# Kernel optimization log

Hardware: AMD Instinct MI355X
Metric: run time of the kernel (lower is better)

Reference implementation:

```python
import jax, jax.numpy as jnp
import numpy as np

C = 512          # channels
NH = 8           # num_heads
ENC = 512        # encoder_channels
SCALE_P = 1.0    # channels_scale_for_positional_embedding
CP = int(C * SCALE_P)
GROUPS = 32


def group_norm(x, g, b, eps=1e-5):
    # x: (N, C, L); GroupNorm32 computes stats in fp32
    N, Ch, L = x.shape
    xg = x.reshape(N, GROUPS, Ch // GROUPS, L).astype(jnp.float32)
    mu = xg.mean(axis=(2, 3), keepdims=True)
    var = xg.var(axis=(2, 3), keepdims=True)
    xn = ((xg - mu) * jax.lax.rsqrt(var + eps)).reshape(N, Ch, L).astype(x.dtype)
    return xn * g[None, :, None] + b[None, :, None]


def conv1(x, W, b):
    # 1x1 conv1d: x (N, Cin, L), W (Cout, Cin), b (Cout)
    return jnp.einsum('oc,ncl->nol', W, x) + b[None, :, None]


def setup_inputs() -> dict:
    key = jax.random.key(0)
    ks = iter(jax.random.split(key, 40))
    rn = lambda *s: jax.random.normal(next(ks), s, dtype=jnp.float32)
    inp = {
        'x': rn(8, C, 32, 32),
        'xf_out': rn(8, ENC, 64),
        'obj_contour_embedding': rn(8, ENC, 64),
        'obj_description_embedding': rn(8, ENC, 64),
        'image_patch_contour_embedding': rn(8, ENC, 1024),
        # norm_for_qkv
        'gn_qkv_g': jnp.ones(C), 'gn_qkv_b': jnp.zeros(C),
        # projectors (1x1 conv weights); zero_module proj_out given random weights for a meaningful baseline
        'W_self_qkv': rn(3 * C, C) * 0.02, 'b_self_qkv': jnp.zeros(3 * C),
        'W_cross_q': rn(C, C) * 0.02, 'b_cross_q': jnp.zeros(C),
        'W_content': rn(2 * C, ENC) * 0.02, 'b_content': jnp.zeros(2 * C),
        'W_pos': rn(CP, ENC) * 0.02, 'b_pos': jnp.zeros(CP),
        'gn_desc_g': jnp.ones(ENC), 'gn_desc_b': jnp.zeros(ENC),
        'gn_cpos_g': jnp.ones(CP), 'gn_cpos_b': jnp.zeros(CP),
        'gn_ipos_g': jnp.ones(CP), 'gn_ipos_b': jnp.zeros(CP),
        'W_self_out': rn(C, C) * 0.02, 'b_self_out': jnp.zeros(C),
        'W_cross_out': rn(C, C) * 0.02, 'b_cross_out': jnp.zeros(C),
    }
    return inp


def _attn(q, k, v, scale):
    # q,k: (B, Cq, T/S), v: (B, Cv, S)
    w = jnp.einsum('bct,bcs->bts', q * scale, k * scale)
    w = jax.nn.softmax(w.astype(jnp.float32), axis=-1).astype(q.dtype)
    return jnp.einsum('bts,bcs->bct', w, v)


def reference(x, xf_out, obj_contour_embedding, obj_description_embedding,
              image_patch_contour_embedding,
              gn_qkv_g, gn_qkv_b, W_self_qkv, b_self_qkv, W_cross_q, b_cross_q,
              W_content, b_content, W_pos, b_pos,
              gn_desc_g, gn_desc_b, gn_cpos_g, gn_cpos_b, gn_ipos_g, gn_ipos_b,
              W_self_out, b_self_out, W_cross_out, b_cross_out):
    b_, c_, h_, w_ = x.shape
    xf = x.reshape(b_, c_, -1)                      # (N, C, L1)
    L1 = xf.shape[-1]
    L2 = obj_contour_embedding.shape[-1]
    dc = C // NH
    dp = CP // NH
    scale = float(int((1 + SCALE_P) * C) // NH) ** -0.25

    # ---- self-attention over image patches ----
    qkv = conv1(group_norm(xf, gn_qkv_g, gn_qkv_b), W_self_qkv, b_self_qkv)
    sq, sk, sv = jnp.split(qkv, 3, axis=1)
    sq = sq.reshape(b_ * NH, dc, L1)
    sk = sk.reshape(b_ * NH, dc, L1)
    sv = sv.reshape(b_ * NH, dc, L1)

    ipos = conv1(image_patch_contour_embedding, W_pos, b_pos)
    ipos = group_norm(ipos, gn_ipos_g, gn_ipos_b)
    ipos = ipos.reshape(b_ * NH, dp, L1)

    sq = jnp.concatenate([sq, ipos], axis=1)
    sk = jnp.concatenate([sk, ipos], axis=1)
    self_out = _attn(sq, sk, sv, scale).reshape(b_, C, L1)
    self_out = conv1(self_out, W_self_out, b_self_out)
    xf = xf + self_out

    # ---- cross-attention to object tokens ----
    cq = conv1(group_norm(xf, gn_qkv_g, gn_qkv_b), W_cross_q, b_cross_q)
    cq = cq.reshape(b_ * NH, dc, L1)
    cq = jnp.concatenate([cq, ipos], axis=1)

    cpos = conv1(obj_contour_embedding, W_pos, b_pos)
    cpos = group_norm(cpos, gn_cpos_g, gn_cpos_b)
    cpos = cpos.reshape(b_ * NH, dp, L2)

    content = (xf_out + group_norm(obj_description_embedding, gn_desc_g, gn_desc_b)) / 2
    kv = conv1(content, W_content, b_content)
    ck, cv = jnp.split(kv, 2, axis=1)
    ck = ck.reshape(b_ * NH, dc, L2)
    cv = cv.reshape(b_ * NH, dc, L2)
    ck = jnp.concatenate([ck, cpos], axis=1)

    cross_out = _attn(cq, ck, cv, scale).reshape(b_, C, L1)
    cross_out = conv1(cross_out, W_cross_out, b_cross_out)

    return (xf + cross_out).reshape(b_, c_, h_, w_)
```

## Files before the change

### kernel.cpp

```cpp
#include <hip/hip_runtime.h>

typedef unsigned short u16;
typedef __attribute__((ext_vector_type(8))) short bf16x8;
typedef __attribute__((ext_vector_type(4))) float f32x4;

__device__ __forceinline__ float bf2f(u16 u) {
  union { unsigned int i; float f; } v;
  v.i = ((unsigned int)u) << 16;
  return v.f;
}
__device__ __forceinline__ u16 f2bf(float f) {
  union { float f; unsigned int i; } v;
  v.f = f;
  unsigned int r = v.i + 0x7FFFu + ((v.i >> 16) & 1u);
  return (u16)(r >> 16);
}
__device__ __forceinline__ unsigned int cvtpk(float lo, float hi) {
  unsigned int r;
  asm("v_cvt_pk_bf16_f32 %0, %1, %2" : "=v"(r) : "v"(lo), "v"(hi));
  return r;
}

__device__ __forceinline__ float4 ld4f(const float* p) {
  return *reinterpret_cast<const float4*>(p);
}
__device__ __forceinline__ float4 ld4f(const u16* p) {
  uint2 v = *reinterpret_cast<const uint2*>(p);
  float4 r;
  r.x = bf2f((u16)(v.x & 0xffff)); r.y = bf2f((u16)(v.x >> 16));
  r.z = bf2f((u16)(v.y & 0xffff)); r.w = bf2f((u16)(v.y >> 16));
  return r;
}

template <typename TIN>
__global__ __launch_bounds__(1024) void gn_kernel(
    const TIN* __restrict__ In, u16* __restrict__ OutBuf,
    const float* __restrict__ G, const float* __restrict__ Bt,
    const float* __restrict__ Add, float post_scale,
    int C, int L, int cpg)
{
  const int blk = blockIdx.x;
  const int n = blk >> 5, grp = blk & 31;
  const size_t base = ((size_t)n * C + (size_t)grp * cpg) * L;
  const int cnt = cpg * L;
  const int cnt4 = cnt >> 2;
  const int tid = threadIdx.x;

  float s = 0.f, s2 = 0.f;
  for (int i = tid; i < cnt4; i += 1024) {
    float4 v = ld4f(In + base + (size_t)i * 4);
    s += v.x + v.y + v.z + v.w;
    s2 += v.x * v.x + v.y * v.y + v.z * v.z + v.w * v.w;
  }
#pragma unroll
  for (int d = 1; d < 64; d <<= 1) {
    s += __shfl_xor(s, d);
    s2 += __shfl_xor(s2, d);
  }
  __shared__ float ps[16], ps2[16], stat[2];
  const int wid = tid >> 6;
  if ((tid & 63) == 0) { ps[wid] = s; ps2[wid] = s2; }
  __syncthreads();
  if (tid == 0) {
    float a = 0.f, b2 = 0.f;
#pragma unroll
    for (int w = 0; w < 16; ++w) { a += ps[w]; b2 += ps2[w]; }
    const float mean = a / cnt;
    const float var = b2 / cnt - mean * mean;
    stat[0] = mean;
    stat[1] = rsqrtf(var + 1e-5f);
  }
  __syncthreads();
  const float mean = stat[0], rstd = stat[1];

  for (int i = tid; i < cnt4; i += 1024) {
    const int i4 = i * 4;
    const int ch = grp * cpg + i4 / L;
    float4 v = ld4f(In + base + i4);
    const float g = G[ch] * rstd, bt = Bt[ch] - mean * rstd * G[ch];
    float4 r;
    r.x = v.x * g + bt; r.y = v.y * g + bt;
    r.z = v.z * g + bt; r.w = v.w * g + bt;
    if (Add) {
      float4 a = *reinterpret_cast<const float4*>(Add + base + i4);
      r.x = (r.x + a.x) * post_scale; r.y = (r.y + a.y) * post_scale;
      r.z = (r.z + a.z) * post_scale; r.w = (r.w + a.w) * post_scale;
    }
    uint2 o;
    o.x = (unsigned int)f2bf(r.x) | ((unsigned int)f2bf(r.y) << 16);
    o.y = (unsigned int)f2bf(r.z) | ((unsigned int)f2bf(r.w) << 16);
    *reinterpret_cast<uint2*>(OutBuf + base + i4) = o;
  }
}

__device__ __forceinline__ void load4(const u16* p, u16* d) {
  uint2 v = *reinterpret_cast<const uint2*>(p);
  d[0] = (u16)(v.x & 0xffff); d[1] = (u16)(v.x >> 16);
  d[2] = (u16)(v.y & 0xffff); d[3] = (u16)(v.y >> 16);
}
__device__ __forceinline__ void load4(const float* p, u16* d) {
  float4 v = *reinterpret_cast<const float4*>(p);
  d[0] = f2bf(v.x); d[1] = f2bf(v.y); d[2] = f2bf(v.z); d[3] = f2bf(v.w);
}
__device__ __forceinline__ void load8(const u16* p, u16* d) {
  union { uint4 q; u16 u[8]; } t;
  t.q = *reinterpret_cast<const uint4*>(p);
#pragma unroll
  for (int i = 0; i < 8; ++i) d[i] = t.u[i];
}

template <typename TX, int LT>
__global__ __launch_bounds__(256) void gemm_conv(
    const TX* __restrict__ X, const float* __restrict__ W,
    const float* __restrict__ Bias,
    u16* __restrict__ OutBf, float* __restrict__ Out32,
    const float* __restrict__ Res,
    int Cin, int L, int O, int mode)
{
  constexpr int NL = LT / 16;
  __shared__ __align__(16) u16 As[64][40];
  __shared__ __align__(16) u16 Bs[LT][40];
  const int tid = threadIdx.x;
  const int wave = tid >> 6;
  const int lane = tid & 63;
  const int n = blockIdx.z;
  const int o0 = blockIdx.x * 64;
  const int l0 = blockIdx.y * LT;
  const TX* Xn = X + (size_t)n * Cin * L;

  const int ao = tid >> 2, akc = (tid & 3) * 8;
  const int c2 = (tid & 15) * 2, lt0 = (tid >> 4) * NL;
  const float* wp = W + (size_t)(o0 + ao) * Cin + akc;
  const TX* xp0 = Xn + (size_t)c2 * L + l0 + lt0;
  const TX* xp1 = xp0 + L;

  f32x4 acc[NL];
#pragma unroll
  for (int i = 0; i < NL; ++i) acc[i] = (f32x4){0.f, 0.f, 0.f, 0.f};

  const int row = lane & 15;
  const int kh = (lane >> 4) * 8;

  float4 wa = *reinterpret_cast<const float4*>(wp);
  float4 wb = *reinterpret_cast<const float4*>(wp + 4);
  u16 blo[NL], bhi[NL];
#pragma unroll
  for (int ch = 0; ch < NL; ch += 4) {
    load4(xp0 + ch, blo + ch);
    load4(xp1 + ch, bhi + ch);
  }

  const int nK = Cin >> 5;
  for (int kt = 0; kt < nK; ++kt) {
    {
      union { uint4 q; u16 u[8]; } ap;
      ap.u[0] = f2bf(wa.x); ap.u[1] = f2bf(wa.y);
      ap.u[2] = f2bf(wa.z); ap.u[3] = f2bf(wa.w);
      ap.u[4] = f2bf(wb.x); ap.u[5] = f2bf(wb.y);
      ap.u[6] = f2bf(wb.z); ap.u[7] = f2bf(wb.w);
      *reinterpret_cast<uint4*>(&As[ao][akc]) = ap.q;
    }
#pragma unroll
    for (int j = 0; j < NL; ++j)
      *reinterpret_cast<unsigned int*>(&Bs[lt0 + j][c2]) =
          (unsigned int)blo[j] | ((unsigned int)bhi[j] << 16);
    __syncthreads();

    if (kt + 1 < nK) {
      const int k0 = (kt + 1) * 32;
      wa = *reinterpret_cast<const float4*>(wp + k0);
      wb = *reinterpret_cast<const float4*>(wp + k0 + 4);
#pragma unroll
      for (int ch = 0; ch < NL; ch += 4) {
        load4(xp0 + (size_t)k0 * L + ch, blo + ch);
        load4(xp1 + (size_t)k0 * L + ch, bhi + ch);
      }
    }

    bf16x8 a = *reinterpret_cast<const bf16x8*>(&As[wave * 16 + row][kh]);
#pragma unroll
    for (int lt = 0; lt < NL; ++lt) {
      bf16x8 b = *reinterpret_cast<const bf16x8*>(&Bs[lt * 16 + row][kh]);
      acc[lt] = __builtin_amdgcn_mfma_f32_16x16x32_bf16(a, b, acc[lt], 0, 0, 0);
    }
    __syncthreads();
  }

  const int col = lane & 15;
  const int r0 = (lane >> 4) * 4;
#pragma unroll
  for (int lt = 0; lt < NL; ++lt) {
    const int ll = l0 + lt * 16 + col;
#pragma unroll
    for (int j = 0; j < 4; ++j) {
      const int oo = o0 + wave * 16 + r0 + j;
      float v = acc[lt][j] + Bias[oo];
      const size_t idx = ((size_t)n * O + oo) * L + ll;
      if (mode == 1) {
        Out32[idx] = v + Res[idx];
      } else {
        OutBf[idx] = f2bf(v);
      }
    }
  }
}

__global__ __launch_bounds__(256) void gemm_qkv(
    const u16* __restrict__ X, const float* __restrict__ W,
    const float* __restrict__ Bias, u16* __restrict__ OutBf,
    int Cin, int L, int O)
{
  __shared__ __align__(16) u16 As[128][40];
  __shared__ __align__(16) u16 Bs[128][40];
  const int tid = threadIdx.x;
  const int wave = tid >> 6;
  const int lane = tid & 63;
  const int n = blockIdx.z;
  const int o0 = blockIdx.x * 128;
  const int l0 = blockIdx.y * 128;
  const u16* Xn = X + (size_t)n * Cin * L;

  const int ao = tid >> 1, ak = (tid & 1) * 16;
  const int c2 = (tid & 15) * 2, lt0 = (tid >> 4) * 8;
  const float* wp = W + (size_t)(o0 + ao) * Cin + ak;
  const u16* xp0 = Xn + (size_t)c2 * L + l0 + lt0;
  const u16* xp1 = xp0 + L;

  f32x4 acc[2][8];
#pragma unroll
  for (int g = 0; g < 2; ++g)
#pragma unroll
    for (int i = 0; i < 8; ++i) acc[g][i] = (f32x4){0.f, 0.f, 0.f, 0.f};

  const int row = lane & 15;
  const int kh = (lane >> 4) * 8;

  float4 w0 = *reinterpret_cast<const float4*>(wp);
  float4 w1 = *reinterpret_cast<const float4*>(wp + 4);
  float4 w2 = *reinterpret_cast<const float4*>(wp + 8);
  float4 w3 = *reinterpret_cast<const float4*>(wp + 12);
  u16 blo[8], bhi[8];
  load8(xp0, blo);
  load8(xp1, bhi);

  const int nK = Cin >> 5;
  for (int kt = 0; kt < nK; ++kt) {
    {
      union { uint4 q; u16 u[8]; } ap;
      ap.u[0] = f2bf(w0.x); ap.u[1] = f2bf(w0.y);
      ap.u[2] = f2bf(w0.z); ap.u[3] = f2bf(w0.w);
      ap.u[4] = f2bf(w1.x); ap.u[5] = f2bf(w1.y);
      ap.u[6] = f2bf(w1.z); ap.u[7] = f2bf(w1.w);
      *reinterpret_cast<uint4*>(&As[ao][ak]) = ap.q;
      ap.u[0] = f2bf(w2.x); ap.u[1] = f2bf(w2.y);
      ap.u[2] = f2bf(w2.z); ap.u[3] = f2bf(w2.w);
      ap.u[4] = f2bf(w3.x); ap.u[5] = f2bf(w3.y);
      ap.u[6] = f2bf(w3.z); ap.u[7] = f2bf(w3.w);
      *reinterpret_cast<uint4*>(&As[ao][ak + 8]) = ap.q;
    }
#pragma unroll
    for (int j = 0; j < 8; ++j)
      *reinterpret_cast<unsigned int*>(&Bs[lt0 + j][c2]) =
          (unsigned int)blo[j] | ((unsigned int)bhi[j] << 16);
    __syncthreads();

    if (kt + 1 < nK) {
      const int k0 = (kt + 1) * 32;
      w0 = *reinterpret_cast<const float4*>(wp + k0);
      w1 = *reinterpret_cast<const float4*>(wp + k0 + 4);
      w2 = *reinterpret_cast<const float4*>(wp + k0 + 8);
      w3 = *reinterpret_cast<const float4*>(wp + k0 + 12);
      load8(xp0 + (size_t)k0 * L, blo);
      load8(xp1 + (size_t)k0 * L, bhi);
    }

    bf16x8 a0 = *reinterpret_cast<const bf16x8*>(&As[wave * 32 + row][kh]);
    bf16x8 a1 = *reinterpret_cast<const bf16x8*>(&As[wave * 32 + 16 + row][kh]);
#pragma unroll
    for (int lt = 0; lt < 8; ++lt) {
      bf16x8 b = *reinterpret_cast<const bf16x8*>(&Bs[lt * 16 + row][kh]);
      acc[0][lt] = __builtin_amdgcn_mfma_f32_16x16x32_bf16(a0, b, acc[0][lt], 0, 0, 0);
      acc[1][lt] = __builtin_amdgcn_mfma_f32_16x16x32_bf16(a1, b, acc[1][lt], 0, 0, 0);
    }
    __syncthreads();
  }

  const int col = lane & 15;
  const int r0 = (lane >> 4) * 4;
#pragma unroll
  for (int g = 0; g < 2; ++g)
#pragma unroll
    for (int lt = 0; lt < 8; ++lt) {
      const int ll = l0 + lt * 16 + col;
#pragma unroll
      for (int j = 0; j < 4; ++j) {
        const int oo = o0 + wave * 32 + g * 16 + r0 + j;
        OutBf[((size_t)n * O + oo) * L + ll] = f2bf(acc[g][lt][j] + Bias[oo]);
      }
    }
}

__global__ __launch_bounds__(256, 2) void flash_attn(
    const u16* __restrict__ qA, int qA_C, int qA_off,
    const u16* __restrict__ qB,
    const u16* __restrict__ kA, int kA_C, int kA_off,
    const u16* __restrict__ kB,
    const u16* __restrict__ V, int v_C, int v_off,
    u16* __restrict__ Out, int S_len, float qscale)
{
  __shared__ __align__(16) u16 smem[20480];
  u16* const Qs = smem;
  u16* const Ks = smem;
  u16* const Ps = smem + 8192;
  u16* const Vt = smem + 16384;

  const int tid = threadIdx.x;
  const int wave = tid >> 6, lane = tid & 63;
  const int b = blockIdx.y >> 3, h = blockIdx.y & 7;
  const int t0 = blockIdx.x * 128;
  const int l16 = lane & 15, q4 = lane >> 4;
  const int swz = (l16 & 7) << 3;

  const int c2 = (tid & 63) * 2;
  const u16* q0 = (c2 < 64)
      ? qA + ((size_t)b * qA_C + qA_off + h * 64 + c2) * 1024 + t0
      : qB + ((size_t)b * 512 + h * 64 + (c2 - 64)) * 1024 + t0;
  const u16* q1 = q0 + 1024;
  const u16* k0 = (c2 < 64)
      ? kA + ((size_t)b * kA_C + kA_off + h * 64 + c2) * (size_t)S_len
      : kB + ((size_t)b * 512 + h * 64 + (c2 - 64)) * (size_t)S_len;
  const u16* k1 = k0 + S_len;
  const u16* vb = V + ((size_t)b * v_C + v_off + h * 64) * (size_t)S_len;

  const int s8 = (tid >> 6) * 8;
  const int cv0 = tid >> 3, sb0 = (tid & 7) * 8;
  const int cv1 = (tid + 256) >> 3, sb1 = sb0;

  uint4 kr0a = *reinterpret_cast<const uint4*>(k0 + s8);
  uint4 kr0c = *reinterpret_cast<const uint4*>(k1 + s8);
  uint4 kr1a = *reinterpret_cast<const uint4*>(k0 + s8 + 32);
  uint4 kr1c = *reinterpret_cast<const uint4*>(k1 + s8 + 32);
  uint4 vr0 = *reinterpret_cast<const uint4*>(vb + (size_t)cv0 * S_len + sb0);
  uint4 vr1 = *reinterpret_cast<const uint4*>(vb + (size_t)cv1 * S_len + sb1);

#pragma unroll
  for (int it = 0; it < 4; ++it) {
    const int t8 = (tid >> 6) * 8 + it * 32;
    union { uint4 q; u16 u[8]; } a, c;
    a.q = *reinterpret_cast<const uint4*>(q0 + t8);
    c.q = *reinterpret_cast<const uint4*>(q1 + t8);
#pragma unroll
    for (int j = 0; j < 8; ++j) {
      const unsigned int w =
          cvtpk(bf2f(a.u[j]) * qscale, bf2f(c.u[j]) * qscale);
      *reinterpret_cast<unsigned int*>(&Qs[(t8 + j) * 128 + (c2 ^ (j << 3))]) = w;
    }
  }
  __syncthreads();

  bf16x8 qf[2][4];
#pragma unroll
  for (int g = 0; g < 2; ++g)
#pragma unroll
    for (int kk = 0; kk < 4; ++kk)
      qf[g][kk] = *reinterpret_cast<const bf16x8*>(
          &Qs[(wave * 32 + g * 16 + l16) * 128 + ((kk * 32 + q4 * 8) ^ swz)]);
  __syncthreads();

  float m_run[2][4], l_run[2][4];
  f32x4 o_acc[2][4];
#pragma unroll
  for (int g = 0; g < 2; ++g)
#pragma unroll
    for (int j = 0; j < 4; ++j) {
      m_run[g][j] = -1e30f; l_run[g][j] = 0.f;
      o_acc[g][j] = (f32x4){0.f, 0.f, 0.f, 0.f};
    }

  const int NT = S_len >> 6;
  for (int t = 0; t < NT; ++t) {
    {
      union { uint4 q; u16 u[8]; } a, c;
      a.q = kr0a; c.q = kr0c;
#pragma unroll
      for (int j = 0; j < 8; ++j)
        *reinterpret_cast<unsigned int*>(&Ks[(s8 + j) * 128 + (c2 ^ (j << 3))]) =
            (unsigned int)a.u[j] | ((unsigned int)c.u[j] << 16);
      a.q = kr1a; c.q = kr1c;
#pragma unroll
      for (int j = 0; j < 8; ++j)
        *reinterpret_cast<unsigned int*>(&Ks[(s8 + 32 + j) * 128 + (c2 ^ (j << 3))]) =
            (unsigned int)a.u[j] | ((unsigned int)c.u[j] << 16);
    }
    *reinterpret_cast<uint4*>(&Vt[cv0 * 64 + (sb0 ^ ((cv0 & 7) << 3))]) = vr0;
    *reinterpret_cast<uint4*>(&Vt[cv1 * 64 + (sb1 ^ ((cv1 & 7) << 3))]) = vr1;
    __syncthreads();

    if (t + 1 < NT) {
      const int sc = (t + 1) * 64;
      kr0a = *reinterpret_cast<const uint4*>(k0 + sc + s8);
      kr0c = *reinterpret_cast<const uint4*>(k1 + sc + s8);
      kr1a = *reinterpret_cast<const uint4*>(k0 + sc + s8 + 32);
      kr1c = *reinterpret_cast<const uint4*>(k1 + sc + s8 + 32);
      vr0 = *reinterpret_cast<const uint4*>(vb + (size_t)cv0 * S_len + sc + sb0);
      vr1 = *reinterpret_cast<const uint4*>(vb + (size_t)cv1 * S_len + sc + sb1);
    }

    f32x4 sacc[2][4];
#pragma unroll
    for (int g = 0; g < 2; ++g)
#pragma unroll
      for (int st = 0; st < 4; ++st) sacc[g][st] = (f32x4){0.f, 0.f, 0.f, 0.f};
    __builtin_amdgcn_s_setprio(1);
#pragma unroll
    for (int st = 0; st < 4; ++st) {
#pragma unroll
      for (int kk = 0; kk < 4; ++kk) {
        bf16x8 kf = *reinterpret_cast<const bf16x8*>(
            &Ks[(st * 16 + l16) * 128 + ((kk * 32 + q4 * 8) ^ swz)]);
        sacc[0][st] = __builtin_amdgcn_mfma_f32_16x16x32_bf16(qf[0][kk], kf, sacc[0][st], 0, 0, 0);
        sacc[1][st] = __builtin_amdgcn_mfma_f32_16x16x32_bf16(qf[1][kk], kf, sacc[1][st], 0, 0, 0);
      }
    }
    __builtin_amdgcn_s_setprio(0);

    float mt[2][4];
#pragma unroll
    for (int g = 0; g < 2; ++g)
#pragma unroll
      for (int j = 0; j < 4; ++j)
        mt[g][j] = fmaxf(fmaxf(sacc[g][0][j], sacc[g][1][j]),
                         fmaxf(sacc[g][2][j], sacc[g][3][j]));

    bool grow = false;
#pragma unroll
    for (int g = 0; g < 2; ++g)
#pragma unroll
      for (int j = 0; j < 4; ++j)
        grow = grow || (mt[g][j] > m_run[g][j] + 8.f);
    if (__any(grow)) {
#pragma unroll
      for (int g = 0; g < 2; ++g) {
#pragma unroll
        for (int d = 1; d < 16; d <<= 1)
#pragma unroll
          for (int j = 0; j < 4; ++j)
            mt[g][j] = fmaxf(mt[g][j], __shfl_xor(mt[g][j], d));
#pragma unroll
        for (int j = 0; j < 4; ++j) {
          const float mn = fmaxf(m_run[g][j], mt[g][j]);
          const float corr = exp2f(m_run[g][j] - mn);
          m_run[g][j] = mn;
          l_run[g][j] *= corr;
#pragma unroll
          for (int ct = 0; ct < 4; ++ct) o_acc[g][ct][j] *= corr;
        }
      }
    }

#pragma unroll
    for (int g = 0; g < 2; ++g)
#pragma unroll
      for (int st = 0; st < 4; ++st)
#pragma unroll
        for (int j = 0; j < 4; ++j) {
          const float p = exp2f(sacc[g][st][j] - m_run[g][j]);
          l_run[g][j] += p;
          Ps[(wave * 32 + g * 16 + q4 * 4 + j) * 64 +
             ((st * 16 + l16) ^ (((q4 * 4 + j) & 7) << 3))] = f2bf(p);
        }

    bf16x8 pa[2][2];
#pragma unroll
    for (int g = 0; g < 2; ++g)
#pragma unroll
      for (int ks = 0; ks < 2; ++ks)
        pa[g][ks] = *reinterpret_cast<const bf16x8*>(
            &Ps[(wave * 32 + g * 16 + l16) * 64 + ((ks * 32 + q4 * 8) ^ swz)]);
    __builtin_amdgcn_s_setprio(1);
#pragma unroll
    for (int ct = 0; ct < 4; ++ct) {
#pragma unroll
      for (int ks = 0; ks < 2; ++ks) {
        bf16x8 vf = *reinterpret_cast<const bf16x8*>(
            &Vt[(ct * 16 + l16) * 64 + ((ks * 32 + q4 * 8) ^ swz)]);
        o_acc[0][ct] = __builtin_amdgcn_mfma_f32_16x16x32_bf16(pa[0][ks], vf, o_acc[0][ct], 0, 0, 0);
        o_acc[1][ct] = __builtin_amdgcn_mfma_f32_16x16x32_bf16(pa[1][ks], vf, o_acc[1][ct], 0, 0, 0);
      }
    }
    __builtin_amdgcn_s_setprio(0);
    __syncthreads();
  }

#pragma unroll
  for (int g = 0; g < 2; ++g) {
#pragma unroll
    for (int d = 1; d < 16; d <<= 1)
#pragma unroll
      for (int j = 0; j < 4; ++j) l_run[g][j] += __shfl_xor(l_run[g][j], d);
    float inv[4];
#pragma unroll
    for (int j = 0; j < 4; ++j) inv[j] = 1.f / l_run[g][j];
    const size_t obase =
        ((size_t)b * 512 + h * 64) * 1024 + t0 + wave * 32 + g * 16 + q4 * 4;
#pragma unroll
    for (int ct = 0; ct < 4; ++ct) {
      union { unsigned long long d; u16 u[4]; } pk;
#pragma unroll
      for (int j = 0; j < 4; ++j) pk.u[j] = f2bf(o_acc[g][ct][j] * inv[j]);
      *reinterpret_cast<unsigned long long*>(
          Out + obase + (size_t)(ct * 16 + l16) * 1024) = pk.d;
    }
  }
}

extern "C" void kernel_launch(void* const* d_in, const int* in_sizes, int n_in,
                              void* d_out, int out_size, void* d_ws, size_t ws_size,
                              hipStream_t stream) {
  const float* X_in        = (const float*)d_in[0];
  const float* xf_out      = (const float*)d_in[1];
  const float* obj_cont    = (const float*)d_in[2];
  const float* obj_desc    = (const float*)d_in[3];
  const float* ipce        = (const float*)d_in[4];
  const float* gn_qkv_g    = (const float*)d_in[5];
  const float* gn_qkv_b    = (const float*)d_in[6];
  const float* W_self_qkv  = (const float*)d_in[7];
  const float* b_self_qkv  = (const float*)d_in[8];
  const float* W_cross_q   = (const float*)d_in[9];
  const float* b_cross_q   = (const float*)d_in[10];
  const float* W_content   = (const float*)d_in[11];
  const float* b_content   = (const float*)d_in[12];
  const float* W_pos       = (const float*)d_in[13];
  const float* b_pos       = (const float*)d_in[14];
  const float* gn_desc_g   = (const float*)d_in[15];
  const float* gn_desc_b   = (const float*)d_in[16];
  const float* gn_cpos_g   = (const float*)d_in[17];
  const float* gn_cpos_b   = (const float*)d_in[18];
  const float* gn_ipos_g   = (const float*)d_in[19];
  const float* gn_ipos_b   = (const float*)d_in[20];
  const float* W_self_out  = (const float*)d_in[21];
  const float* b_self_out  = (const float*)d_in[22];
  const float* W_cross_out = (const float*)d_in[23];
  const float* b_cross_out = (const float*)d_in[24];

  char* base = (char*)d_ws;
  u16* A = (u16*)base;
  u16* B = (u16*)(base + 8 * 1024 * 1024);
  u16* C = (u16*)(base + 32 * 1024 * 1024);
  u16* D = (u16*)(base + 40 * 1024 * 1024);

  u16* norm1 = A;
  u16* norm2 = A;
  u16* cposr   = A;
  u16* cpos    = A + 262144;
  u16* content = A + 2 * 262144;
  u16* kvbuf   = A + 3 * 262144;
  u16* qkv  = B;
  u16* cq   = B;
  u16* ipos = C;
  u16* iposr = D;
  u16* attn1 = D;
  u16* cattn = D;
  float* xf32 = (float*)d_out;
  float* outp = (float*)d_out;

  const float qscale = 0.08838834764831845f * 1.4426950408889634f;
  dim3 blk(256);
  dim3 blkgn(1024);

  gn_kernel<float><<<dim3(256), blkgn, 0, stream>>>(X_in, norm1, gn_qkv_g, gn_qkv_b,
                                                    nullptr, 1.f, 512, 1024, 16);
  gemm_qkv<<<dim3(12, 8, 8), blk, 0, stream>>>(norm1, W_self_qkv, b_self_qkv,
                                               qkv, 512, 1024, 1536);
  gemm_conv<float, 128><<<dim3(8, 8, 8), blk, 0, stream>>>(ipce, W_pos, b_pos, iposr,
                                                           nullptr, nullptr,
                                                           512, 1024, 512, 0);
  gn_kernel<u16><<<dim3(256), blkgn, 0, stream>>>(iposr, ipos, gn_ipos_g, gn_ipos_b,
                                                  nullptr, 1.f, 512, 1024, 16);
  flash_attn<<<dim3(8, 64), blk, 0, stream>>>(qkv, 1536, 0, ipos,
                                              qkv, 1536, 512, ipos,
                                              qkv, 1536, 1024,
                                              attn1, 1024, qscale);
  gemm_conv<u16, 128><<<dim3(8, 8, 8), blk, 0, stream>>>(attn1, W_self_out, b_self_out,
                                                         nullptr, xf32, X_in,
                                                         512, 1024, 512, 1);
  gn_kernel<float><<<dim3(256), blkgn, 0, stream>>>(xf32, norm2, gn_qkv_g, gn_qkv_b,
                                                    nullptr, 1.f, 512, 1024, 16);
  gemm_conv<u16, 128><<<dim3(8, 8, 8), blk, 0, stream>>>(norm2, W_cross_q, b_cross_q, cq,
                                                         nullptr, nullptr,
                                                         512, 1024, 512, 0);
  gemm_conv<float, 64><<<dim3(8, 1, 8), blk, 0, stream>>>(obj_cont, W_pos, b_pos, cposr,
                                                          nullptr, nullptr,
                                                          512, 64, 512, 0);
  gn_kernel<u16><<<dim3(256), blkgn, 0, stream>>>(cposr, cpos, gn_cpos_g, gn_cpos_b,
                                                  nullptr, 1.f, 512, 64, 16);
  gn_kernel<float><<<dim3(256), blkgn, 0, stream>>>(obj_desc, content, gn_desc_g,
                                                    gn_desc_b, xf_out, 0.5f, 512, 64, 16);
  gemm_conv<u16, 64><<<dim3(16, 1, 8), blk, 0, stream>>>(content, W_content, b_content,
                                                         kvbuf, nullptr, nullptr,
                                                         512, 64, 1024, 0);
  flash_attn<<<dim3(8, 64), blk, 0, stream>>>(cq, 512, 0, ipos,
                                              kvbuf, 1024, 0, cpos,
                                              kvbuf, 1024, 512,
                                              cattn, 64, qscale);
  gemm_conv<u16, 128><<<dim3(8, 8, 8), blk, 0, stream>>>(cattn, W_cross_out, b_cross_out,
                                                         nullptr, outp, xf32,
                                                         512, 1024, 512, 1);
}
```

Measured before the change: 247.8 us.

## Use 512-thread flash attention blocks with one 16-row query group per wave

The flash attention kernel moves from 4 waves each owning 32 query rows to 8 waves each owning 16 rows, with 512 threads per block. The K, V and Q staging loads are spread over more threads, so each thread loads half as much. Per-thread register use for the accumulators and Q fragments roughly halves, which gives more waves in flight to hide latency. In exchange, each K/V fragment read from shared memory now feeds one MFMA instead of two, and more waves take part in each block barrier.

```diff
diff --git a/kernel.cpp b/kernel.cpp
--- a/kernel.cpp
+++ b/kernel.cpp
@@ -300,7 +300,7 @@
     }
 }
 
-__global__ __launch_bounds__(256, 2) void flash_attn(
+__global__ __launch_bounds__(512) void flash_attn(
     const u16* __restrict__ qA, int qA_C, int qA_off,
     const u16* __restrict__ qB,
     const u16* __restrict__ kA, int kA_C, int kA_off,
@@ -321,7 +321,7 @@
   const int l16 = lane & 15, q4 = lane >> 4;
   const int swz = (l16 & 7) << 3;
 
-  const int c2 = (tid & 63) * 2;
+  const int c2 = lane * 2;
   const u16* q0 = (c2 < 64)
       ? qA + ((size_t)b * qA_C + qA_off + h * 64 + c2) * 1024 + t0
       : qB + ((size_t)b * 512 + h * 64 + (c2 - 64)) * 1024 + t0;
@@ -332,20 +332,16 @@
   const u16* k1 = k0 + S_len;
   const u16* vb = V + ((size_t)b * v_C + v_off + h * 64) * (size_t)S_len;
 
-  const int s8 = (tid >> 6) * 8;
-  const int cv0 = tid >> 3, sb0 = (tid & 7) * 8;
-  const int cv1 = (tid + 256) >> 3, sb1 = sb0;
-
-  uint4 kr0a = *reinterpret_cast<const uint4*>(k0 + s8);
-  uint4 kr0c = *reinterpret_cast<const uint4*>(k1 + s8);
-  uint4 kr1a = *reinterpret_cast<const uint4*>(k0 + s8 + 32);
-  uint4 kr1c = *reinterpret_cast<const uint4*>(k1 + s8 + 32);
-  uint4 vr0 = *reinterpret_cast<const uint4*>(vb + (size_t)cv0 * S_len + sb0);
-  uint4 vr1 = *reinterpret_cast<const uint4*>(vb + (size_t)cv1 * S_len + sb1);
-
-#pragma unroll
-  for (int it = 0; it < 4; ++it) {
-    const int t8 = (tid >> 6) * 8 + it * 32;
+  const int s8 = wave * 8;
+  const int cv = tid >> 3, sb = (tid & 7) * 8;
+
+  uint4 kra = *reinterpret_cast<const uint4*>(k0 + s8);
+  uint4 krc = *reinterpret_cast<const uint4*>(k1 + s8);
+  uint4 vr = *reinterpret_cast<const uint4*>(vb + (size_t)cv * S_len + sb);
+
+#pragma unroll
+  for (int it = 0; it < 2; ++it) {
+    const int t8 = wave * 8 + it * 64;
     union { uint4 q; u16 u[8]; } a, c;
     a.q = *reinterpret_cast<const uint4*>(q0 + t8);
     c.q = *reinterpret_cast<const uint4*>(q1 + t8);
@@ -358,59 +354,44 @@
   }
   __syncthreads();
 
-  bf16x8 qf[2][4];
-#pragma unroll
-  for (int g = 0; g < 2; ++g)
-#pragma unroll
-    for (int kk = 0; kk < 4; ++kk)
-      qf[g][kk] = *reinterpret_cast<const bf16x8*>(
-          &Qs[(wave * 32 + g * 16 + l16) * 128 + ((kk * 32 + q4 * 8) ^ swz)]);
+  bf16x8 qf[4];
+#pragma unroll
+  for (int kk = 0; kk < 4; ++kk)
+    qf[kk] = *reinterpret_cast<const bf16x8*>(
+        &Qs[(wave * 16 + l16) * 128 + ((kk * 32 + q4 * 8) ^ swz)]);
   __syncthreads();
 
-  float m_run[2][4], l_run[2][4];
-  f32x4 o_acc[2][4];
-#pragma unroll
-  for (int g = 0; g < 2; ++g)
-#pragma unroll
-    for (int j = 0; j < 4; ++j) {
-      m_run[g][j] = -1e30f; l_run[g][j] = 0.f;
-      o_acc[g][j] = (f32x4){0.f, 0.f, 0.f, 0.f};
-    }
+  float m_run[4], l_run[4];
+  f32x4 o_acc[4];
+#pragma unroll
+  for (int j = 0; j < 4; ++j) {
+    m_run[j] = -1e30f; l_run[j] = 0.f;
+    o_acc[j] = (f32x4){0.f, 0.f, 0.f, 0.f};
+  }
 
   const int NT = S_len >> 6;
   for (int t = 0; t < NT; ++t) {
     {
       union { uint4 q; u16 u[8]; } a, c;
-      a.q = kr0a; c.q = kr0c;
+      a.q = kra; c.q = krc;
 #pragma unroll
       for (int j = 0; j < 8; ++j)
         *reinterpret_cast<unsigned int*>(&Ks[(s8 + j) * 128 + (c2 ^ (j << 3))]) =
             (unsigned int)a.u[j] | ((unsigned int)c.u[j] << 16);
-      a.q = kr1a; c.q = kr1c;
-#pragma unroll
-      for (int j = 0; j < 8; ++j)
-        *reinterpret_cast<unsigned int*>(&Ks[(s8 + 32 + j) * 128 + (c2 ^ (j << 3))]) =
-            (unsigned int)a.u[j] | ((unsigned int)c.u[j] << 16);
-    }
-    *reinterpret_cast<uint4*>(&Vt[cv0 * 64 + (sb0 ^ ((cv0 & 7) << 3))]) = vr0;
-    *reinterpret_cast<uint4*>(&Vt[cv1 * 64 + (sb1 ^ ((cv1 & 7) << 3))]) = vr1;
+    }
+    *reinterpret_cast<uint4*>(&Vt[cv * 64 + (sb ^ ((cv & 7) << 3))]) = vr;
     __syncthreads();
 
     if (t + 1 < NT) {
       const int sc = (t + 1) * 64;
-      kr0a = *reinterpret_cast<const uint4*>(k0 + sc + s8);
-      kr0c = *reinterpret_cast<const uint4*>(k1 + sc + s8);
-      kr1a = *reinterpret_cast<const uint4*>(k0 + sc + s8 + 32);
-      kr1c = *reinterpret_cast<const uint4*>(k1 + sc + s8 + 32);
-      vr0 = *reinterpret_cast<const uint4*>(vb + (size_t)cv0 * S_len + sc + sb0);
-      vr1 = *reinterpret_cast<const uint4*>(vb + (size_t)cv1 * S_len + sc + sb1);
-    }
-
-    f32x4 sacc[2][4];
-#pragma unroll
-    for (int g = 0; g < 2; ++g)
-#pragma unroll
-      for (int st = 0; st < 4; ++st) sacc[g][st] = (f32x4){0.f, 0.f, 0.f, 0.f};
+      kra = *reinterpret_cast<const uint4*>(k0 + sc + s8);
+      krc = *reinterpret_cast<const uint4*>(k1 + sc + s8);
+      vr = *reinterpret_cast<const uint4*>(vb + (size_t)cv * S_len + sc + sb);
+    }
+
+    f32x4 sacc[4];
+#pragma unroll
+    for (int st = 0; st < 4; ++st) sacc[st] = (f32x4){0.f, 0.f, 0.f, 0.f};
     __builtin_amdgcn_s_setprio(1);
 #pragma unroll
     for (int st = 0; st < 4; ++st) {
@@ -418,65 +399,53 @@
       for (int kk = 0; kk < 4; ++kk) {
         bf16x8 kf = *reinterpret_cast<const bf16x8*>(
             &Ks[(st * 16 + l16) * 128 + ((kk * 32 + q4 * 8) ^ swz)]);
-        sacc[0][st] = __builtin_amdgcn_mfma_f32_16x16x32_bf16(qf[0][kk], kf, sacc[0][st], 0, 0, 0);
-        sacc[1][st] = __builtin_amdgcn_mfma_f32_16x16x32_bf16(qf[1][kk], kf, sacc[1][st], 0, 0, 0);
+        sacc[st] = __builtin_amdgcn_mfma_f32_16x16x32_bf16(qf[kk], kf, sacc[st], 0, 0, 0);
       }
     }
     __builtin_amdgcn_s_setprio(0);
 
-    float mt[2][4];
-#pragma unroll
-    for (int g = 0; g < 2; ++g)
-#pragma unroll
-      for (int j = 0; j < 4; ++j)
-        mt[g][j] = fmaxf(fmaxf(sacc[g][0][j], sacc[g][1][j]),
-                         fmaxf(sacc[g][2][j], sacc[g][3][j]));
+    float mt[4];
+#pragma unroll
+    for (int j = 0; j < 4; ++j)
+      mt[j] = fmaxf(fmaxf(sacc[0][j], sacc[1][j]),
+                    fmaxf(sacc[2][j], sacc[3][j]));
 
     bool grow = false;
 #pragma unroll
-    for (int g = 0; g < 2; ++g)
-#pragma unroll
-      for (int j = 0; j < 4; ++j)
-        grow = grow || (mt[g][j] > m_run[g][j] + 8.f);
+    for (int j = 0; j < 4; ++j)
+      grow = grow || (mt[j] > m_run[j] + 8.f);
     if (__any(grow)) {
 #pragma unroll
-      for (int g = 0; g < 2; ++g) {
-#pragma unroll
-        for (int d = 1; d < 16; d <<= 1)
-#pragma unroll
-          for (int j = 0; j < 4; ++j)
-            mt[g][j] = fmaxf(mt[g][j], __shfl_xor(mt[g][j], d));
-#pragma unroll
-        for (int j = 0; j < 4; ++j) {
-          const float mn = fmaxf(m_run[g][j], mt[g][j]);
-          const float corr = exp2f(m_run[g][j] - mn);
-          m_run[g][j] = mn;
-          l_run[g][j] *= corr;
-#pragma unroll
-          for (int ct = 0; ct < 4; ++ct) o_acc[g][ct][j] *= corr;
-        }
-      }
-    }
-
-#pragma unroll
-    for (int g = 0; g < 2; ++g)
-#pragma unroll
-      for (int st = 0; st < 4; ++st)
-#pragma unroll
-        for (int j = 0; j < 4; ++j) {
-          const float p = exp2f(sacc[g][st][j] - m_run[g][j]);
-          l_run[g][j] += p;
-          Ps[(wave * 32 + g * 16 + q4 * 4 + j) * 64 +
-             ((st * 16 + l16) ^ (((q4 * 4 + j) & 7) << 3))] = f2bf(p);
-        }
-
-    bf16x8 pa[2][2];
-#pragma unroll
-    for (int g = 0; g < 2; ++g)
-#pragma unroll
-      for (int ks = 0; ks < 2; ++ks)
-        pa[g][ks] = *reinterpret_cast<const bf16x8*>(
-            &Ps[(wave * 32 + g * 16 + l16) * 64 + ((ks * 32 + q4 * 8) ^ swz)]);
+      for (int d = 1; d < 16; d <<= 1)
+#pragma unroll
+        for (int j = 0; j < 4; ++j)
+          mt[j] = fmaxf(mt[j], __shfl_xor(mt[j], d));
+#pragma unroll
+      for (int j = 0; j < 4; ++j) {
+        const float mn = fmaxf(m_run[j], mt[j]);
+        const float corr = exp2f(m_run[j] - mn);
+        m_run[j] = mn;
+        l_run[j] *= corr;
+#pragma unroll
+        for (int ct = 0; ct < 4; ++ct) o_acc[ct][j] *= corr;
+      }
+    }
+
+#pragma unroll
+    for (int st = 0; st < 4; ++st)
+#pragma unroll
+      for (int j = 0; j < 4; ++j) {
+        const float p = exp2f(sacc[st][j] - m_run[j]);
+        l_run[j] += p;
+        Ps[(wave * 16 + q4 * 4 + j) * 64 +
+           ((st * 16 + l16) ^ (((q4 * 4 + j) & 7) << 3))] = f2bf(p);
+      }
+
+    bf16x8 pa[2];
+#pragma unroll
+    for (int ks = 0; ks < 2; ++ks)
+      pa[ks] = *reinterpret_cast<const bf16x8*>(
+          &Ps[(wave * 16 + l16) * 64 + ((ks * 32 + q4 * 8) ^ swz)]);
     __builtin_amdgcn_s_setprio(1);
 #pragma unroll
     for (int ct = 0; ct < 4; ++ct) {
@@ -484,8 +453,7 @@
       for (int ks = 0; ks < 2; ++ks) {
         bf16x8 vf = *reinterpret_cast<const bf16x8*>(
             &Vt[(ct * 16 + l16) * 64 + ((ks * 32 + q4 * 8) ^ swz)]);
-        o_acc[0][ct] = __builtin_amdgcn_mfma_f32_16x16x32_bf16(pa[0][ks], vf, o_acc[0][ct], 0, 0, 0);
-        o_acc[1][ct] = __builtin_amdgcn_mfma_f32_16x16x32_bf16(pa[1][ks], vf, o_acc[1][ct], 0, 0, 0);
+        o_acc[ct] = __builtin_amdgcn_mfma_f32_16x16x32_bf16(pa[ks], vf, o_acc[ct], 0, 0, 0);
       }
     }
     __builtin_amdgcn_s_setprio(0);
@@ -493,24 +461,21 @@
   }
 
 #pragma unroll
-  for (int g = 0; g < 2; ++g) {
-#pragma unroll
-    for (int d = 1; d < 16; d <<= 1)
-#pragma unroll
-      for (int j = 0; j < 4; ++j) l_run[g][j] += __shfl_xor(l_run[g][j], d);
-    float inv[4];
-#pragma unroll
-    for (int j = 0; j < 4; ++j) inv[j] = 1.f / l_run[g][j];
-    const size_t obase =
-        ((size_t)b * 512 + h * 64) * 1024 + t0 + wave * 32 + g * 16 + q4 * 4;
-#pragma unroll
-    for (int ct = 0; ct < 4; ++ct) {
-      union { unsigned long long d; u16 u[4]; } pk;
-#pragma unroll
-      for (int j = 0; j < 4; ++j) pk.u[j] = f2bf(o_acc[g][ct][j] * inv[j]);
-      *reinterpret_cast<unsigned long long*>(
-          Out + obase + (size_t)(ct * 16 + l16) * 1024) = pk.d;
-    }
+  for (int d = 1; d < 16; d <<= 1)
+#pragma unroll
+    for (int j = 0; j < 4; ++j) l_run[j] += __shfl_xor(l_run[j], d);
+  float inv[4];
+#pragma unroll
+  for (int j = 0; j < 4; ++j) inv[j] = 1.f / l_run[j];
+  const size_t obase =
+      ((size_t)b * 512 + h * 64) * 1024 + t0 + wave * 16 + q4 * 4;
+#pragma unroll
+  for (int ct = 0; ct < 4; ++ct) {
+    union { unsigned long long d; u16 u[4]; } pk;
+#pragma unroll
+    for (int j = 0; j < 4; ++j) pk.u[j] = f2bf(o_acc[ct][j] * inv[j]);
+    *reinterpret_cast<unsigned long long*>(
+        Out + obase + (size_t)(ct * 16 + l16) * 1024) = pk.d;
   }
 }
 
@@ -566,6 +531,7 @@
 
   const float qscale = 0.08838834764831845f * 1.4426950408889634f;
   dim3 blk(256);
+  dim3 blkf(512);
   dim3 blkgn(1024);
 
   gn_kernel<float><<<dim3(256), blkgn, 0, stream>>>(X_in, norm1, gn_qkv_g, gn_qkv_b,
@@ -577,10 +543,10 @@
                                                            512, 1024, 512, 0);
   gn_kernel<u16><<<dim3(256), blkgn, 0, stream>>>(iposr, ipos, gn_ipos_g, gn_ipos_b,
                                                   nullptr, 1.f, 512, 1024, 16);
-  flash_attn<<<dim3(8, 64), blk, 0, stream>>>(qkv, 1536, 0, ipos,
-                                              qkv, 1536, 512, ipos,
-                                              qkv, 1536, 1024,
-                                              attn1, 1024, qscale);
+  flash_attn<<<dim3(8, 64), blkf, 0, stream>>>(qkv, 1536, 0, ipos,
+                                               qkv, 1536, 512, ipos,
+                                               qkv, 1536, 1024,
+                                               attn1, 1024, qscale);
   gemm_conv<u16, 128><<<dim3(8, 8, 8), blk, 0, stream>>>(attn1, W_self_out, b_self_out,
                                                          nullptr, xf32, X_in,
                                                          512, 1024, 512, 1);
@@ -599,10 +565,10 @@
   gemm_conv<u16, 64><<<dim3(16, 1, 8), blk, 0, stream>>>(content, W_content, b_content,
                                                          kvbuf, nullptr, nullptr,
                                                          512, 64, 1024, 0);
-  flash_attn<<<dim3(8, 64), blk, 0, stream>>>(cq, 512, 0, ipos,
-                                              kvbuf, 1024, 0, cpos,
-                                              kvbuf, 1024, 512,
-                                              cattn, 64, qscale);
+  flash_attn<<<dim3(8, 64), blkf, 0, stream>>>(cq, 512, 0, ipos,
+                                               kvbuf, 1024, 0, cpos,
+                                               kvbuf, 1024, 512,
+                                               cattn, 64, qscale);
   gemm_conv<u16, 128><<<dim3(8, 8, 8), blk, 0, stream>>>(cattn, W_cross_out, b_cross_out,
                                                          nullptr, outp, xf32,
                                                          512, 1024, 512, 1);
```

After: 268.8 us. +8.5%, slower.
